# Optimization experiments

Measured on AMD Instinct MI355X. Metric: run time of the kernel, lower is better.

## Reference

```python
import jax, jax.numpy as jnp
import numpy as np

D_MODEL = 1024
N_HEADS = 16
HEAD_DIM = D_MODEL // N_HEADS
WINDOW = 256


def setup_inputs() -> dict:
    key = jax.random.key(0)
    k1, k2, k3 = jax.random.split(key, 3)
    x = jax.random.normal(k1, (1, 4096, D_MODEL), dtype=jnp.float32)
    # torch nn.Linear weights: [out_features, in_features]
    W_qkv = jax.random.normal(k2, (3 * D_MODEL, D_MODEL), dtype=jnp.float32) * (D_MODEL ** -0.5)
    W_proj = jax.random.normal(k3, (D_MODEL, D_MODEL), dtype=jnp.float32) * (D_MODEL ** -0.5)
    return {"x": x, "W_qkv": W_qkv, "W_proj": W_proj}


def reference(x, W_qkv, W_proj):
    B, T, D = x.shape
    H, Hd = N_HEADS, HEAD_DIM
    qkv = (x @ W_qkv.T).reshape(B, T, 3, H, Hd)
    qkv = jnp.transpose(qkv, (2, 0, 3, 1, 4))  # [3, B, H, T, Hd]
    q, k, v = qkv[0], qkv[1], qkv[2]
    # causal + sliding-window mask: allowed iff 0 <= i - j < WINDOW
    i = jnp.arange(T)[:, None]
    j = jnp.arange(T)[None, :]
    mask = (j <= i) & (j >= i - (WINDOW - 1))  # [T, T] bool
    scale = Hd ** -0.5
    attn = jnp.einsum('bhid,bhjd->bhij', q, k) * scale
    attn = jnp.where(mask, attn, -jnp.inf)
    attn = jax.nn.softmax(attn, axis=-1)
    out = jnp.einsum('bhij,bhjd->bhid', attn, v)  # [B, H, T, Hd]
    out = jnp.transpose(out, (0, 2, 1, 3)).reshape(B, T, D)
    return out @ W_proj.T
```

## Files before the change

kernel.cpp:

```cpp
#include <hip/hip_runtime.h>
#include <hip/hip_bf16.h>


#define T_SEQ   4096
#define DM      1024
#define NH      16
#define HD      64
#define WIN     256

typedef unsigned short u16_t;
typedef u16_t  u16v8 __attribute__((ext_vector_type(8)));
typedef __bf16 bf16v8 __attribute__((ext_vector_type(8)));
typedef float  f32v4 __attribute__((ext_vector_type(4)));

__device__ __forceinline__ f32v4 mfma_bf16(u16v8 a, u16v8 b, f32v4 c) {
    return __builtin_amdgcn_mfma_f32_16x16x32_bf16(
        __builtin_bit_cast(bf16v8, a), __builtin_bit_cast(bf16v8, b), c, 0, 0, 0);
}

__device__ __forceinline__ u16_t f2bf(float f) {
    unsigned u = __builtin_bit_cast(unsigned, f);
    u += 0x7fffu + ((u >> 16) & 1u);
    return (u16_t)(u >> 16);
}

__device__ __forceinline__ float exp2_fast(float x) {
    return __builtin_amdgcn_exp2f(x);
}

__device__ __forceinline__ void gload_lds16(const u16_t* g, u16_t* l) {
    __builtin_amdgcn_global_load_lds(
        (const __attribute__((address_space(1))) unsigned int*)g,
        (__attribute__((address_space(3))) unsigned int*)l, 16, 0, 0);
}

__global__ void cvt_kernel(const float* __restrict__ in, u16_t* __restrict__ out, int n8) {
    int i = blockIdx.x * blockDim.x + threadIdx.x;
    if (i >= n8) return;
    const float4* p = (const float4*)(in + (size_t)i * 8);
    float4 a = p[0], b = p[1];
    u16v8 o;
    o[0] = f2bf(a.x); o[1] = f2bf(a.y); o[2] = f2bf(a.z); o[3] = f2bf(a.w);
    o[4] = f2bf(b.x); o[5] = f2bf(b.y); o[6] = f2bf(b.z); o[7] = f2bf(b.w);
    *(u16v8*)(out + (size_t)i * 8) = o;
}

template <int BM, int BN, int WN, int WAVES, int MW, typename OutT>
__global__ __launch_bounds__(WAVES * 64, MW)
void gemm2p(const u16_t* __restrict__ A, const u16_t* __restrict__ B,
            OutT* __restrict__ C, int M, int N, int K) {
    constexpr int WM  = WAVES / WN;
    constexpr int PWM = BM / WM;
    constexpr int PWN = BN / WN;
    constexpr int M_F = PWM / 16, N_F = PWN / 16;
    constexpr int THREADS = WAVES * 64;
    constexpr int RPP = THREADS / 4;

    __shared__ u16_t lA[2][BM * 32];
    __shared__ u16_t lB[2][BN * 32];

    const int tid = threadIdx.x;
    const int l = tid & 63, w = tid >> 6;
    const int lr = l & 15, g = l >> 4;
    const int wrh = w / WN, wcq = w % WN;
    const int arow0 = blockIdx.y * BM, bcol0 = blockIdx.x * BN;
    const int rq = tid >> 2, cq = tid & 3;
    const int NT = K >> 5;

    f32v4 acc[M_F][N_F];
#pragma unroll
    for (int m = 0; m < M_F; ++m)
#pragma unroll
        for (int n = 0; n < N_F; ++n) acc[m][n] = f32v4{0.f, 0.f, 0.f, 0.f};

#define GSTAGE(buf, kt0)                                                                \
    do {                                                                                \
        _Pragma("unroll")                                                               \
        for (int p = 0; p < BM / RPP; ++p) {                                            \
            int r = rq + p * RPP;                                                       \
            int cs = cq ^ ((r >> 1) & 3);                                               \
            gload_lds16(A + (size_t)(arow0 + r) * K + (kt0) + cs * 8,                   \
                        lA[buf] + r * 32 + cq * 8);                                     \
        }                                                                               \
        _Pragma("unroll")                                                               \
        for (int p = 0; p < BN / RPP; ++p) {                                            \
            int r = rq + p * RPP;                                                       \
            int cs = cq ^ ((r >> 1) & 3);                                               \
            gload_lds16(B + (size_t)(bcol0 + r) * K + (kt0) + cs * 8,                   \
                        lB[buf] + r * 32 + cq * 8);                                     \
        }                                                                               \
    } while (0)

    GSTAGE(0, 0);
    __syncthreads();

    for (int t = 0; t < NT; ++t) {
        if (t + 1 < NT) GSTAGE((t + 1) & 1, (t + 1) << 5);
        __builtin_amdgcn_sched_barrier(0);

        const u16_t* sA = lA[t & 1];
        const u16_t* sB = lB[t & 1];
        u16v8 a[M_F], b[N_F];
#pragma unroll
        for (int mf = 0; mf < M_F; ++mf) {
            int row = wrh * PWM + mf * 16 + lr;
            a[mf] = *(const u16v8*)(sA + row * 32 + (g ^ ((row >> 1) & 3)) * 8);
        }
#pragma unroll
        for (int nf = 0; nf < N_F; ++nf) {
            int row = wcq * PWN + nf * 16 + lr;
            b[nf] = *(const u16v8*)(sB + row * 32 + (g ^ ((row >> 1) & 3)) * 8);
        }
        __builtin_amdgcn_s_setprio(1);
#pragma unroll
        for (int mf = 0; mf < M_F; ++mf)
#pragma unroll
            for (int nf = 0; nf < N_F; ++nf)
                acc[mf][nf] = mfma_bf16(a[mf], b[nf], acc[mf][nf]);
        __builtin_amdgcn_s_setprio(0);

        __syncthreads();
    }
#undef GSTAGE

#pragma unroll
    for (int mf = 0; mf < M_F; ++mf) {
        int crow0 = arow0 + wrh * PWM + mf * 16 + g * 4;
#pragma unroll
        for (int nf = 0; nf < N_F; ++nf) {
            int ccol = bcol0 + wcq * PWN + nf * 16 + lr;
#pragma unroll
            for (int j = 0; j < 4; ++j) {
                float v = acc[mf][nf][j];
                if constexpr (sizeof(OutT) == 2)
                    C[(size_t)(crow0 + j) * N + ccol] = (OutT)f2bf(v);
                else
                    C[(size_t)(crow0 + j) * N + ccol] = (OutT)v;
            }
        }
    }
}

__global__ __launch_bounds__(256) void vtrans_kernel(const u16_t* __restrict__ qkv,
                                                     u16_t* __restrict__ vt) {
    __shared__ u16_t tile[64][72];
    const int t0 = blockIdx.x * 64, h = blockIdx.y;
    const int tid = threadIdx.x;
    {
        int r = tid >> 2, c = (tid & 3) * 16;
        const u16_t* src = qkv + (size_t)(t0 + r) * (3 * DM) + 2 * DM + h * HD + c;
        *(u16v8*)&tile[r][c]     = *(const u16v8*)src;
        *(u16v8*)&tile[r][c + 8] = *(const u16v8*)(src + 8);
    }
    __syncthreads();
    {
        int d = tid >> 2, ts = (tid & 3) * 16;
        u16_t* dst = vt + ((size_t)h * HD + d) * T_SEQ + t0 + ts;
        u16v8 o0, o1;
#pragma unroll
        for (int i = 0; i < 8; ++i) { o0[i] = tile[ts + i][d]; o1[i] = tile[ts + 8 + i][d]; }
        *(u16v8*)dst       = o0;
        *(u16v8*)(dst + 8) = o1;
    }
}

__global__ __launch_bounds__(256) void attn_kernel(const u16_t* __restrict__ qkv,
                                                   const u16_t* __restrict__ vt,
                                                   u16_t* __restrict__ out) {
    __shared__ u16_t lK[2][64 * 64];
    __shared__ u16_t lV[2][64 * 64];
    __shared__ u16_t pbuf[4][16 * 64];

    const int h = blockIdx.y;
    const int q0 = blockIdx.x * 64;
    const int tid = threadIdx.x;
    const int w = tid >> 6, l = tid & 63;
    const int lr = l & 15, g = l >> 4;
    const int i0 = q0 + w * 16;
    u16_t* P = pbuf[w];

    const int r_st = tid >> 3;
    const int c8l  = tid & 7;
    const u16_t* kBase = qkv + DM + h * HD;
    const u16_t* vBase = vt + (size_t)h * HD * T_SEQ;

    u16v8 qf0, qf1;
    {
        const u16_t* qrow = qkv + h * HD + (size_t)(i0 + lr) * (3 * DM) + g * 8;
        qf0 = *(const u16v8*)qrow;
        qf1 = *(const u16v8*)(qrow + 32);
    }
    f32v4 o[4];
#pragma unroll
    for (int n = 0; n < 4; ++n) o[n] = f32v4{0.f, 0.f, 0.f, 0.f};
    float m_run[4], l_run[4];
#pragma unroll
    for (int j = 0; j < 4; ++j) { m_run[j] = -1e30f; l_run[j] = 0.f; }

    const int c0 = (q0 >= WIN) ? q0 - WIN : 0;
    const int nch = ((q0 - c0) >> 6) + 1;

#define STAGE_KV(buf, cc)                                                              \
    do {                                                                               \
        _Pragma("unroll")                                                              \
        for (int p = 0; p < 2; ++p) {                                                  \
            int rr = r_st + p * 32;                                                    \
            int cs = c8l ^ (rr & 7);                                                   \
            gload_lds16(kBase + (size_t)(cc + rr) * (3 * DM) + cs * 8,                 \
                        lK[buf] + (size_t)(rr * 64 + c8l * 8));                        \
            gload_lds16(vBase + (size_t)rr * T_SEQ + (cc) + cs * 8,                    \
                        lV[buf] + (size_t)(rr * 64 + c8l * 8));                        \
        }                                                                              \
    } while (0)

    STAGE_KV(0, c0);

    const float sc = 0.125f * 1.4426950408889634f;

    for (int ci = 0; ci < nch; ++ci) {
        const int c = c0 + (ci << 6);
        const int cur = ci & 1;
        __syncthreads();
        if (ci + 1 < nch) STAGE_KV(cur ^ 1, c + 64);

        const u16_t* K = lK[cur];
        const u16_t* V = lV[cur];

        f32v4 s[4];
#pragma unroll
        for (int kt = 0; kt < 4; ++kt) {
            int krow = kt * 16 + lr;
            u16v8 k0 = *(const u16v8*)(K + krow * 64 + ((g     ^ (krow & 7)) * 8));
            u16v8 k1 = *(const u16v8*)(K + krow * 64 + (((4+g) ^ (krow & 7)) * 8));
            f32v4 z = f32v4{0.f, 0.f, 0.f, 0.f};
            z = mfma_bf16(qf0, k0, z);
            z = mfma_bf16(qf1, k1, z);
            s[kt] = z;
        }

        const bool full = (c + 63 <= i0) && (c >= i0 - 240);
        if (full) {
#pragma unroll
            for (int kt = 0; kt < 4; ++kt)
#pragma unroll
                for (int j = 0; j < 4; ++j) s[kt][j] *= sc;
        } else {
#pragma unroll
            for (int j = 0; j < 4; ++j) {
                const int i = i0 + g * 4 + j;
#pragma unroll
                for (int kt = 0; kt < 4; ++kt) {
                    const int jg = c + kt * 16 + lr;
                    float v = s[kt][j] * sc;
                    const bool okm = (jg <= i) && (jg >= i - (WIN - 1));
                    s[kt][j] = okm ? v : -3e38f;
                }
            }
        }

        float mloc[4], corr[4], rsum[4];
#pragma unroll
        for (int j = 0; j < 4; ++j)
            mloc[j] = fmaxf(fmaxf(s[0][j], s[1][j]), fmaxf(s[2][j], s[3][j]));
#pragma unroll
        for (int d = 1; d < 16; d <<= 1)
#pragma unroll
            for (int j = 0; j < 4; ++j) mloc[j] = fmaxf(mloc[j], __shfl_xor(mloc[j], d, 64));
#pragma unroll
        for (int j = 0; j < 4; ++j) {
            float mnew = fmaxf(m_run[j], mloc[j]);
            corr[j] = exp2_fast(m_run[j] - mnew);
            m_run[j] = mnew;
            rsum[j] = 0.f;
        }
#pragma unroll
        for (int kt = 0; kt < 4; ++kt)
#pragma unroll
            for (int j = 0; j < 4; ++j) {
                float p = exp2_fast(s[kt][j] - m_run[j]);
                rsum[j] += p;
                int rP = g * 4 + j;
                int col = kt * 16 + lr;
                int c8 = col >> 3;
                P[rP * 64 + ((c8 ^ (rP & 7)) * 8 + (col & 7))] = f2bf(p);
            }
#pragma unroll
        for (int d = 1; d < 16; d <<= 1)
#pragma unroll
            for (int j = 0; j < 4; ++j) rsum[j] += __shfl_xor(rsum[j], d, 64);
#pragma unroll
        for (int j = 0; j < 4; ++j) l_run[j] = l_run[j] * corr[j] + rsum[j];
#pragma unroll
        for (int n = 0; n < 4; ++n)
#pragma unroll
            for (int j = 0; j < 4; ++j) o[n][j] *= corr[j];

        u16v8 pa0 = *(const u16v8*)(P + lr * 64 + ((g     ^ (lr & 7)) * 8));
        u16v8 pa1 = *(const u16v8*)(P + lr * 64 + (((4+g) ^ (lr & 7)) * 8));
#pragma unroll
        for (int n = 0; n < 4; ++n) {
            int vrow = n * 16 + lr;
            u16v8 v0 = *(const u16v8*)(V + vrow * 64 + ((g     ^ (vrow & 7)) * 8));
            u16v8 v1 = *(const u16v8*)(V + vrow * 64 + (((4+g) ^ (vrow & 7)) * 8));
            o[n] = mfma_bf16(pa0, v0, o[n]);
            o[n] = mfma_bf16(pa1, v1, o[n]);
        }
    }
#undef STAGE_KV

#pragma unroll
    for (int n = 0; n < 4; ++n)
#pragma unroll
        for (int j = 0; j < 4; ++j) {
            int t = i0 + g * 4 + j;
            out[(size_t)t * DM + h * HD + n * 16 + lr] = f2bf(o[n][j] / l_run[j]);
        }
}

extern "C" void kernel_launch(void* const* d_in, const int* in_sizes, int n_in,
                              void* d_out, int out_size, void* d_ws, size_t ws_size,
                              hipStream_t stream) {
    const float* x     = (const float*)d_in[0];
    const float* wqkv  = (const float*)d_in[1];
    const float* wproj = (const float*)d_in[2];
    float* out = (float*)d_out;
    char* ws = (char*)d_ws;

    u16_t* xb     = (u16_t*)(ws);
    u16_t* wqkvb  = (u16_t*)(ws + (size_t)(8u << 20));
    u16_t* wprojb = (u16_t*)(ws + (size_t)(14u << 20));
    u16_t* qkvb   = (u16_t*)(ws + (size_t)(16u << 20));
    u16_t* vt     = (u16_t*)(ws + (size_t)(40u << 20));
    u16_t* attnb  = (u16_t*)(ws);

    const int n8x = T_SEQ * DM / 8, n8q = 3 * DM * DM / 8, n8p = DM * DM / 8;
    cvt_kernel<<<(n8x + 255) / 256, 256, 0, stream>>>(x, xb, n8x);
    cvt_kernel<<<(n8q + 255) / 256, 256, 0, stream>>>(wqkv, wqkvb, n8q);
    cvt_kernel<<<(n8p + 255) / 256, 256, 0, stream>>>(wproj, wprojb, n8p);

    gemm2p<128, 128, 2, 4, 3, u16_t><<<dim3(3 * DM / 128, T_SEQ / 128), 256, 0, stream>>>(
        xb, wqkvb, qkvb, T_SEQ, 3 * DM, DM);

    vtrans_kernel<<<dim3(T_SEQ / 64, NH), 256, 0, stream>>>(qkvb, vt);

    attn_kernel<<<dim3(T_SEQ / 64, NH), 256, 0, stream>>>(qkvb, vt, attnb);

    gemm2p<64, 128, 2, 4, 2, float><<<dim3(DM / 128, T_SEQ / 64), 256, 0, stream>>>(
        attnb, wprojb, out, T_SEQ, DM, DM);
}
```

Before: 165.1 us.

## Fuse V transpose into QKV GEMM epilogue and merge conversion kernels

The three fp32-to-bf16 conversion launches are merged into one kernel that dispatches by global index. The separate V-transpose kernel is removed: QKV GEMM tiles covering the V columns now write their accumulators directly in transposed [h*HD+d][T] layout with 4-element vector stores. This removes two kernel launches and the extra read/write pass over V, at the cost of scattered 8-byte stores in the GEMM epilogue and no longer writing V into the qkv buffer.

```diff
diff --git a/kernel.cpp b/kernel.cpp
--- a/kernel.cpp
+++ b/kernel.cpp
@@ -9,6 +9,7 @@
 #define WIN     256
 
 typedef unsigned short u16_t;
+typedef u16_t  u16v4 __attribute__((ext_vector_type(4)));
 typedef u16_t  u16v8 __attribute__((ext_vector_type(8)));
 typedef __bf16 bf16v8 __attribute__((ext_vector_type(8)));
 typedef float  f32v4 __attribute__((ext_vector_type(4)));
@@ -34,21 +35,29 @@
         (__attribute__((address_space(3))) unsigned int*)l, 16, 0, 0);
 }
 
-__global__ void cvt_kernel(const float* __restrict__ in, u16_t* __restrict__ out, int n8) {
+#define N8X (T_SEQ * DM / 8)
+#define N8Q (3 * DM * DM / 8)
+#define N8P (DM * DM / 8)
+__global__ void cvt3_kernel(const float* __restrict__ x, const float* __restrict__ wqkv,
+                            const float* __restrict__ wproj, u16_t* __restrict__ xb,
+                            u16_t* __restrict__ wqkvb, u16_t* __restrict__ wprojb) {
     int i = blockIdx.x * blockDim.x + threadIdx.x;
-    if (i >= n8) return;
-    const float4* p = (const float4*)(in + (size_t)i * 8);
+    const float* src; u16_t* dst; int off;
+    if (i < N8X)            { src = x;     dst = xb;     off = i; }
+    else if (i < N8X + N8Q) { src = wqkv;  dst = wqkvb;  off = i - N8X; }
+    else                    { src = wproj; dst = wprojb; off = i - N8X - N8Q; }
+    const float4* p = (const float4*)(src + (size_t)off * 8);
     float4 a = p[0], b = p[1];
     u16v8 o;
     o[0] = f2bf(a.x); o[1] = f2bf(a.y); o[2] = f2bf(a.z); o[3] = f2bf(a.w);
     o[4] = f2bf(b.x); o[5] = f2bf(b.y); o[6] = f2bf(b.z); o[7] = f2bf(b.w);
-    *(u16v8*)(out + (size_t)i * 8) = o;
-}
-
-template <int BM, int BN, int WN, int WAVES, int MW, typename OutT>
+    *(u16v8*)(dst + (size_t)off * 8) = o;
+}
+
+template <int BM, int BN, int WN, int WAVES, int MW, bool VT, typename OutT>
 __global__ __launch_bounds__(WAVES * 64, MW)
 void gemm2p(const u16_t* __restrict__ A, const u16_t* __restrict__ B,
-            OutT* __restrict__ C, int M, int N, int K) {
+            OutT* __restrict__ C, u16_t* __restrict__ vtp, int M, int N, int K) {
     constexpr int WM  = WAVES / WN;
     constexpr int PWM = BM / WM;
     constexpr int PWN = BN / WN;
@@ -123,44 +132,36 @@
     }
 #undef GSTAGE
 
-#pragma unroll
-    for (int mf = 0; mf < M_F; ++mf) {
-        int crow0 = arow0 + wrh * PWM + mf * 16 + g * 4;
-#pragma unroll
-        for (int nf = 0; nf < N_F; ++nf) {
-            int ccol = bcol0 + wcq * PWN + nf * 16 + lr;
-#pragma unroll
-            for (int j = 0; j < 4; ++j) {
-                float v = acc[mf][nf][j];
-                if constexpr (sizeof(OutT) == 2)
-                    C[(size_t)(crow0 + j) * N + ccol] = (OutT)f2bf(v);
-                else
-                    C[(size_t)(crow0 + j) * N + ccol] = (OutT)v;
+    if (VT && bcol0 >= 2 * DM) {
+#pragma unroll
+        for (int mf = 0; mf < M_F; ++mf) {
+            int crow0 = arow0 + wrh * PWM + mf * 16 + g * 4;
+#pragma unroll
+            for (int nf = 0; nf < N_F; ++nf) {
+                int ccol = bcol0 + wcq * PWN + nf * 16 + lr;
+                u16v4 v4;
+#pragma unroll
+                for (int j = 0; j < 4; ++j) v4[j] = f2bf(acc[mf][nf][j]);
+                *(u16v4*)(vtp + (size_t)(ccol - 2 * DM) * T_SEQ + crow0) = v4;
             }
         }
-    }
-}
-
-__global__ __launch_bounds__(256) void vtrans_kernel(const u16_t* __restrict__ qkv,
-                                                     u16_t* __restrict__ vt) {
-    __shared__ u16_t tile[64][72];
-    const int t0 = blockIdx.x * 64, h = blockIdx.y;
-    const int tid = threadIdx.x;
-    {
-        int r = tid >> 2, c = (tid & 3) * 16;
-        const u16_t* src = qkv + (size_t)(t0 + r) * (3 * DM) + 2 * DM + h * HD + c;
-        *(u16v8*)&tile[r][c]     = *(const u16v8*)src;
-        *(u16v8*)&tile[r][c + 8] = *(const u16v8*)(src + 8);
-    }
-    __syncthreads();
-    {
-        int d = tid >> 2, ts = (tid & 3) * 16;
-        u16_t* dst = vt + ((size_t)h * HD + d) * T_SEQ + t0 + ts;
-        u16v8 o0, o1;
-#pragma unroll
-        for (int i = 0; i < 8; ++i) { o0[i] = tile[ts + i][d]; o1[i] = tile[ts + 8 + i][d]; }
-        *(u16v8*)dst       = o0;
-        *(u16v8*)(dst + 8) = o1;
+    } else {
+#pragma unroll
+        for (int mf = 0; mf < M_F; ++mf) {
+            int crow0 = arow0 + wrh * PWM + mf * 16 + g * 4;
+#pragma unroll
+            for (int nf = 0; nf < N_F; ++nf) {
+                int ccol = bcol0 + wcq * PWN + nf * 16 + lr;
+#pragma unroll
+                for (int j = 0; j < 4; ++j) {
+                    float v = acc[mf][nf][j];
+                    if constexpr (sizeof(OutT) == 2)
+                        C[(size_t)(crow0 + j) * N + ccol] = (OutT)f2bf(v);
+                    else
+                        C[(size_t)(crow0 + j) * N + ccol] = (OutT)v;
+                }
+            }
+        }
     }
 }
 
@@ -333,18 +334,14 @@
     u16_t* vt     = (u16_t*)(ws + (size_t)(40u << 20));
     u16_t* attnb  = (u16_t*)(ws);
 
-    const int n8x = T_SEQ * DM / 8, n8q = 3 * DM * DM / 8, n8p = DM * DM / 8;
-    cvt_kernel<<<(n8x + 255) / 256, 256, 0, stream>>>(x, xb, n8x);
-    cvt_kernel<<<(n8q + 255) / 256, 256, 0, stream>>>(wqkv, wqkvb, n8q);
-    cvt_kernel<<<(n8p + 255) / 256, 256, 0, stream>>>(wproj, wprojb, n8p);
-
-    gemm2p<128, 128, 2, 4, 3, u16_t><<<dim3(3 * DM / 128, T_SEQ / 128), 256, 0, stream>>>(
-        xb, wqkvb, qkvb, T_SEQ, 3 * DM, DM);
-
-    vtrans_kernel<<<dim3(T_SEQ / 64, NH), 256, 0, stream>>>(qkvb, vt);
+    cvt3_kernel<<<(N8X + N8Q + N8P + 255) / 256, 256, 0, stream>>>(
+        x, wqkv, wproj, xb, wqkvb, wprojb);
+
+    gemm2p<128, 128, 2, 4, 3, true, u16_t><<<dim3(3 * DM / 128, T_SEQ / 128), 256, 0, stream>>>(
+        xb, wqkvb, qkvb, vt, T_SEQ, 3 * DM, DM);
 
     attn_kernel<<<dim3(T_SEQ / 64, NH), 256, 0, stream>>>(qkvb, vt, attnb);
 
-    gemm2p<64, 128, 2, 4, 2, float><<<dim3(DM / 128, T_SEQ / 64), 256, 0, stream>>>(
-        attnb, wprojb, out, T_SEQ, DM, DM);
-}
+    gemm2p<64, 128, 2, 4, 2, false, float><<<dim3(DM / 128, T_SEQ / 64), 256, 0, stream>>>(
+        attnb, wprojb, out, nullptr, T_SEQ, DM, DM);
+}
```

New measurement: 158.2 us. 4.2% less time.
